# Optimization experiments

Hardware: AMD Instinct MI355X
Metric: run time of the kernel (lower is better)

Reference implementation:

```python
import jax, jax.numpy as jnp
import numpy as np
from jax import lax

B, N = 4, 192
D_IN = 768       # bert hidden
H = 512          # lstm_hid_size (bidirectional)
HD = H // 2
DIST_E = 20
TYPE_E = 20
CONV_IN = H + DIST_E + TYPE_E   # 552
CONV_H = 96
DILATIONS = (1, 2, 3)
BIAFF = 512
CLS = 10
N_POS = 30
SIZE_E = 25


def setup_inputs() -> dict:
    key = jax.random.key(0)
    ks = iter(jax.random.split(key, 48))

    def nrm(shape, s):
        return jax.random.normal(next(ks), shape, jnp.float32) * s

    word_reps = jax.random.normal(next(ks), (B, N, D_IN), jnp.float32)
    word_length = jnp.concatenate([
        jnp.array([N], jnp.int32),
        jax.random.randint(next(ks), (B - 1,), N // 2, N + 1).astype(jnp.int32)])
    dist_inputs = jax.random.randint(next(ks), (B, N, N), 0, 20)
    ar = jnp.arange(N)
    valid = (ar[None, :, None] < word_length[:, None, None]) & (ar[None, None, :] < word_length[:, None, None])
    loss_mask = valid.astype(jnp.int32)
    return dict(
        word_reps=word_reps, word_length=word_length, dist_inputs=dist_inputs, loss_mask=loss_mask,
        lstm_Wih_f=nrm((4 * HD, D_IN), 0.03), lstm_Whh_f=nrm((4 * HD, HD), 0.03), lstm_b_f=jnp.zeros((4 * HD,), jnp.float32),
        lstm_Wih_b=nrm((4 * HD, D_IN), 0.03), lstm_Whh_b=nrm((4 * HD, HD), 0.03), lstm_b_b=jnp.zeros((4 * HD,), jnp.float32),
        cln_gamma=jnp.ones((H,), jnp.float32), cln_beta=jnp.zeros((H,), jnp.float32),
        cln_Wg=nrm((H, H), 0.02), cln_Wb=nrm((H, H), 0.02),
        dis_emb=nrm((20, DIST_E), 0.1), reg_emb=nrm((3, TYPE_E), 0.1),
        conv_base_w=nrm((1, 1, CONV_IN, CONV_H), 0.05), conv_base_b=jnp.zeros((CONV_H,), jnp.float32),
        conv_dw_w=nrm((len(DILATIONS), 3, 3, 1, CONV_H), 0.05), conv_dw_b=jnp.zeros((len(DILATIONS), CONV_H), jnp.float32),
        mlp1_w=nrm((BIAFF, H), 0.04), mlp1_b=jnp.zeros((BIAFF,), jnp.float32),
        mlp2_w=nrm((BIAFF, H), 0.04), mlp2_b=jnp.zeros((BIAFF,), jnp.float32),
        head_w=nrm((BIAFF, H), 0.04), head_b=jnp.zeros((BIAFF,), jnp.float32),
        tail_w=nrm((BIAFF, H), 0.04), tail_b=jnp.zeros((BIAFF,), jnp.float32),
        biaff_W=nrm((CLS, BIAFF + 1, BIAFF + 1), 0.02),
        size_emb=nrm((N_POS, SIZE_E), 0.1),
        W_co=nrm((CLS, 2 * (BIAFF + 1) + SIZE_E), 0.02),
    )


def _lstm_dir(x, mask, Wih, Whh, b):
    # x: [B,T,D], mask: [B,T] bool. PyTorch LSTM (packed): padded steps emit 0, state frozen.
    xw = jnp.einsum('btd,gd->btg', x, Wih) + b  # precomputed input projection, gate order i,f,g,o
    h0 = jnp.zeros((x.shape[0], Whh.shape[1]), x.dtype)

    def step(carry, inp):
        h, c = carry
        xw_t, m_t = inp
        gates = xw_t + h @ Whh.T
        i, f, g, o = jnp.split(gates, 4, axis=-1)
        c_new = jax.nn.sigmoid(f) * c + jax.nn.sigmoid(i) * jnp.tanh(g)
        h_new = jax.nn.sigmoid(o) * jnp.tanh(c_new)
        m = m_t[:, None]
        h = jnp.where(m, h_new, h)
        c = jnp.where(m, c_new, c)
        return (h, c), jnp.where(m, h_new, 0.0)

    _, hs = lax.scan(step, (h0, h0), (xw.transpose(1, 0, 2), mask.T))
    return hs.transpose(1, 0, 2)


def _conv2d_nhwc(x, w, b, dil, groups):
    pad = (w.shape[0] - 1) // 2 * dil
    y = lax.conv_general_dilated(
        x, w, window_strides=(1, 1), padding=[(pad, pad), (pad, pad)],
        rhs_dilation=(dil, dil),
        dimension_numbers=('NHWC', 'HWIO', 'NHWC'),
        feature_group_count=groups)
    return y + b


def _forward(word_reps, lstm_Wih_f, lstm_Whh_f, lstm_b_f, lstm_Wih_b, lstm_Whh_b, lstm_b_b,
             cln_gamma, cln_beta, cln_Wg, cln_Wb, dis_emb, reg_emb,
             conv_base_w, conv_base_b, conv_dw_w, conv_dw_b,
             mlp1_w, mlp1_b, mlp2_w, mlp2_b, head_w, head_b, tail_w, tail_b,
             biaff_W, size_emb, W_co,
             word_length, dist_inputs, loss_mask):
    Bsz, T, _ = word_reps.shape
    ar = jnp.arange(T)
    seq_mask = ar[None, :] < word_length[:, None]

    # --- BiLSTM over packed (length-masked) sequences ---
    fwd = _lstm_dir(word_reps, seq_mask, lstm_Wih_f, lstm_Whh_f, lstm_b_f)
    idx = jnp.clip(word_length[:, None] - 1 - ar[None, :], 0, T - 1)  # reverse within each length
    x_rev = jnp.take_along_axis(word_reps, idx[:, :, None], axis=1)
    bwd_rev = _lstm_dir(x_rev, seq_mask, lstm_Wih_b, lstm_Whh_b, lstm_b_b)
    bwd = jnp.take_along_axis(bwd_rev, idx[:, :, None], axis=1) * seq_mask[:, :, None]
    wr = jnp.concatenate([fwd, bwd], axis=-1)  # [B,T,H]

    # --- conditional LayerNorm: normalize wr[i], scale/shift conditioned on wr[j] ---
    mu = wr.mean(-1, keepdims=True)
    xc = wr - mu
    var = (xc * xc).mean(-1, keepdims=True)
    ln = xc / jnp.sqrt(var + 1e-12)                 # [B,T,H]
    w_cond = cln_gamma + wr @ cln_Wg.T              # [B,T,H]
    b_cond = cln_beta + wr @ cln_Wb.T
    cln = ln[:, :, None, :] * w_cond[:, None, :, :] + b_cond[:, None, :, :]  # [B,T,T,H]

    dis = dis_emb[dist_inputs]                      # [B,T,T,20]
    reg_inputs = jnp.tril(loss_mask) + loss_mask    # values in {0,1,2}
    reg = reg_emb[reg_inputs]                       # [B,T,T,20]
    grid_mask = (loss_mask != 0)[..., None]
    conv_in = jnp.where(grid_mask, jnp.concatenate([dis, reg, cln], axis=-1), 0.0)

    # --- dilated depthwise conv stack (act='leakyrelu') ---
    x = jax.nn.leaky_relu(_conv2d_nhwc(conv_in, conv_base_w, conv_base_b, 1, 1))
    outs = []
    for i, d in enumerate(DILATIONS):
        x = jax.nn.leaky_relu(_conv2d_nhwc(x, conv_dw_w[i], conv_dw_b[i], d, CONV_H))
        outs.append(x)
    conv_out = jnp.where(grid_mask, jnp.concatenate(outs, axis=-1), 0.0)
    del conv_out  # computed in source, but CoPredictor.forward ignores z (faithful)

    # --- CoPredictor ---
    gelu = lambda v: jax.nn.gelu(v, approximate=False)
    h = gelu(wr @ mlp1_w.T + mlp1_b)
    t = gelu(wr @ mlp2_w.T + mlp2_b)
    ones = jnp.ones(h.shape[:-1] + (1,), h.dtype)
    h1 = jnp.concatenate([h, ones], -1)
    t1 = jnp.concatenate([t, ones], -1)
    o1 = jnp.einsum('bxi,oij,byj->bxyo', h1, biaff_W, t1)  # [B,T,T,CLS]

    head = jnp.concatenate([jax.nn.leaky_relu(wr @ head_w.T + head_b), ones], -1)  # [B,T,P]
    tail = jnp.concatenate([jax.nn.leaky_relu(wr @ tail_w.T + tail_b), ones], -1)
    span = ar[None, :] - ar[:, None]
    span = jnp.clip(span, -(N_POS // 2), N_POS // 2 - 1) + N_POS // 2
    se = size_emb[span]  # [T,T,SIZE_E]
    P = BIAFF + 1
    # einsum over the concat [head|tail|size] split into three partial products (no [B,T,T,1051] materialization)
    o3 = (jnp.einsum('bmi,ki->bkm', head, W_co[:, :P])[:, :, :, None]
          + jnp.einsum('bni,ki->bkn', tail, W_co[:, P:2 * P])[:, :, None, :]
          + jnp.einsum('mns,ks->kmn', se, W_co[:, 2 * P:])[None])
    return jnp.transpose(o1, (0, 3, 1, 2)) + o3  # [B,CLS,T,T]


def reference(word_reps, word_length, dist_inputs, loss_mask,
              lstm_Wih_f, lstm_Whh_f, lstm_b_f, lstm_Wih_b, lstm_Whh_b, lstm_b_b,
              cln_gamma, cln_beta, cln_Wg, cln_Wb, dis_emb, reg_emb,
              conv_base_w, conv_base_b, conv_dw_w, conv_dw_b,
              mlp1_w, mlp1_b, mlp2_w, mlp2_b, head_w, head_b, tail_w, tail_b,
              biaff_W, size_emb, W_co):
    return _forward(word_reps, lstm_Wih_f, lstm_Whh_f, lstm_b_f, lstm_Wih_b, lstm_Whh_b, lstm_b_b,
                    cln_gamma, cln_beta, cln_Wg, cln_Wb, dis_emb, reg_emb,
                    conv_base_w, conv_base_b, conv_dw_w, conv_dw_b,
                    mlp1_w, mlp1_b, mlp2_w, mlp2_b, head_w, head_b, tail_w, tail_b,
                    biaff_W, size_emb, W_co,
                    word_length, dist_inputs, loss_mask)
```

## Files before the change

kernel.cpp:

```cpp
#include <hip/hip_runtime.h>
#include <math.h>

#define BB 4
#define NN 192
#define DIN 768
#define HD 256
#define HH 512
#define PP 513
#define CLS 10
#define NBIG 5130
#define KP 544
#define WCO_LD 1051
#define LMAX 192

typedef __attribute__((ext_vector_type(8))) __bf16 bf16x8;
typedef __attribute__((ext_vector_type(4))) float f32x4;
typedef unsigned short u16;
typedef unsigned long long u64;

__device__ __forceinline__ float sigf(float x) { return 1.f / (1.f + expf(-x)); }

__device__ __forceinline__ u16 f2bf(float f) {
    unsigned int x = __float_as_uint(f);
    unsigned int r = (x + 0x7FFF + ((x >> 16) & 1)) >> 16;
    return (u16)r;
}
__device__ __forceinline__ float bf2f(u16 h) {
    return __uint_as_float(((unsigned int)h) << 16);
}

__global__ void split_hl(const float* __restrict__ src, u16* __restrict__ hi,
                         u16* __restrict__ lo, int n)
{
    int i = blockIdx.x * blockDim.x + threadIdx.x;
    if (i >= n) return;
    float v = src[i];
    u16 h = f2bf(v);
    hi[i] = h;
    lo[i] = f2bf(v - bf2f(h));
}

__global__ void split_ht(const float* __restrict__ HT, u16* __restrict__ h1h,
                         u16* __restrict__ h1l, u16* __restrict__ t1h,
                         u16* __restrict__ t1l)
{
    int idx = blockIdx.x * blockDim.x + threadIdx.x;
    if (idx >= 768 * KP) return;
    int m = idx / KP, k = idx - m * KP;
    float hv = (k < 512) ? HT[(size_t)m * 2048 + k] : (k == 512 ? 1.f : 0.f);
    float tv = (k < 512) ? HT[(size_t)m * 2048 + 512 + k] : (k == 512 ? 1.f : 0.f);
    u16 hh = f2bf(hv);
    h1h[idx] = hh; h1l[idx] = f2bf(hv - bf2f(hh));
    u16 th = f2bf(tv);
    t1h[idx] = th; t1l[idx] = f2bf(tv - bf2f(th));
}

__global__ void wsplit_kernel(const float* __restrict__ W, u16* __restrict__ Wh,
                              u16* __restrict__ Wl)
{
    __shared__ float tile[32][33];
    int kc = blockIdx.z, k0 = blockIdx.x * 32, j0 = blockIdx.y * 32;
    int tx = threadIdx.x, ty = threadIdx.y;
#pragma unroll
    for (int yy = 0; yy < 32; yy += 8) {
        int k = k0 + ty + yy, j = j0 + tx;
        tile[ty + yy][tx] = (k < 513 && j < 513) ? W[((size_t)kc * 513 + k) * 513 + j] : 0.f;
    }
    __syncthreads();
#pragma unroll
    for (int yy = 0; yy < 32; yy += 8) {
        int j = j0 + ty + yy, k = k0 + tx;
        if (j < 513 && k < KP) {
            float v = tile[tx][ty + yy];
            size_t o = ((size_t)kc * 513 + j) * KP + k;
            u16 h = f2bf(v);
            Wh[o] = h; Wl[o] = f2bf(v - bf2f(h));
        }
    }
}

__global__ __launch_bounds__(256)
void gemm_mfma_hl(const u16* __restrict__ Ah, const u16* __restrict__ Al,
                  const u16* __restrict__ Bh, const u16* __restrict__ Bl,
                  const float* __restrict__ bias, float* __restrict__ C,
                  int K, int ldc, int act)
{
    const int lane = threadIdx.x & 63, w = threadIdx.x >> 6;
    const int m0 = blockIdx.y * 64;
    const int n0 = blockIdx.x * 64 + w * 16;
    const int arow = m0 + (lane & 15);
    const int brow = n0 + (lane & 15);
    const int koff = (lane >> 4) * 8;
    f32x4 acc[4] = {};

    for (int k0 = 0; k0 < K; k0 += 32) {
        bf16x8 bh = *(const bf16x8*)(Bh + (size_t)brow * K + k0 + koff);
        bf16x8 bl = *(const bf16x8*)(Bl + (size_t)brow * K + k0 + koff);
#pragma unroll
        for (int mi = 0; mi < 4; ++mi) {
            size_t ao = (size_t)(arow + mi * 16) * K + k0 + koff;
            bf16x8 ah = *(const bf16x8*)(Ah + ao);
            bf16x8 al = *(const bf16x8*)(Al + ao);
            acc[mi] = __builtin_amdgcn_mfma_f32_16x16x32_bf16(ah, bh, acc[mi], 0, 0, 0);
            acc[mi] = __builtin_amdgcn_mfma_f32_16x16x32_bf16(ah, bl, acc[mi], 0, 0, 0);
            acc[mi] = __builtin_amdgcn_mfma_f32_16x16x32_bf16(al, bh, acc[mi], 0, 0, 0);
        }
    }
    const float bv = bias ? bias[n0 + (lane & 15)] : 0.f;
    const int cn = n0 + (lane & 15);
#pragma unroll
    for (int mi = 0; mi < 4; ++mi)
#pragma unroll
        for (int r = 0; r < 4; ++r) {
            int m = m0 + mi * 16 + (lane >> 4) * 4 + r;
            float v = acc[mi][r] + bv;
            if (act == 1) v = 0.5f * v * (1.f + erff(v * 0.70710678118654752f));
            else if (act == 2) v = v > 0.f ? v : 0.01f * v;
            C[(size_t)m * ldc + cn] = v;
        }
}

__global__ __launch_bounds__(256)
void biaff_mfma(const u16* __restrict__ Ah, const u16* __restrict__ Al,
                const u16* __restrict__ Wh, const u16* __restrict__ Wl,
                u16* __restrict__ Mh, u16* __restrict__ Ml)
{
    const int lane = threadIdx.x & 63, w = threadIdx.x >> 6;
    const int m0 = blockIdx.y * 64;
    const int n0 = blockIdx.x * 128 + w * 32;
    const int arow = m0 + (lane & 15);
    const int koff = (lane >> 4) * 8;
    f32x4 acc[4][2] = {};

    for (int c = 0; c < 17; ++c) {
        const int k0 = c * 32 + koff;
        bf16x8 bh[2], bl[2];
#pragma unroll
        for (int ni = 0; ni < 2; ++ni) {
            size_t bo = (size_t)(n0 + ni * 16 + (lane & 15)) * KP + k0;
            bh[ni] = *(const bf16x8*)(Wh + bo);
            bl[ni] = *(const bf16x8*)(Wl + bo);
        }
#pragma unroll
        for (int mi = 0; mi < 4; ++mi) {
            size_t ao = (size_t)(arow + mi * 16) * KP + k0;
            bf16x8 ah = *(const bf16x8*)(Ah + ao);
            bf16x8 al = *(const bf16x8*)(Al + ao);
#pragma unroll
            for (int ni = 0; ni < 2; ++ni) {
                acc[mi][ni] = __builtin_amdgcn_mfma_f32_16x16x32_bf16(ah, bh[ni], acc[mi][ni], 0, 0, 0);
                acc[mi][ni] = __builtin_amdgcn_mfma_f32_16x16x32_bf16(ah, bl[ni], acc[mi][ni], 0, 0, 0);
                acc[mi][ni] = __builtin_amdgcn_mfma_f32_16x16x32_bf16(al, bh[ni], acc[mi][ni], 0, 0, 0);
            }
        }
    }
#pragma unroll
    for (int mi = 0; mi < 4; ++mi)
#pragma unroll
        for (int ni = 0; ni < 2; ++ni) {
            int n = n0 + ni * 16 + (lane & 15);
            if (n < NBIG) {
                int kc = n / PP, j = n - kc * PP;
#pragma unroll
                for (int r = 0; r < 4; ++r) {
                    int m = m0 + mi * 16 + (lane >> 4) * 4 + r;
                    float v = acc[mi][ni][r];
                    u16 h = f2bf(v);
                    size_t o = (size_t)m * (CLS * KP) + kc * KP + j;
                    Mh[o] = h; Ml[o] = f2bf(v - bf2f(h));
                }
            }
        }
}

__global__ __launch_bounds__(256)
void final_mfma(const u16* __restrict__ Mh, const u16* __restrict__ Ml,
                const u16* __restrict__ Th, const u16* __restrict__ Tl,
                const float* __restrict__ hv, const float* __restrict__ tv,
                const float* __restrict__ Tt, float* __restrict__ out)
{
    const int lane = threadIdx.x & 63, w = threadIdx.x >> 6;
    const int r0 = blockIdx.y * 64;
    const int b = r0 / 1920;
    const int rem = r0 - b * 1920;
    const int kc = rem / 192;
    const int x0 = rem - kc * 192;
    const int n0 = blockIdx.x * 64 + w * 16;
    const int koff = (lane >> 4) * 8;
    const size_t abase = (size_t)(b * 192 + x0 + (lane & 15)) * (CLS * KP) + kc * KP;
    const size_t bbase = (size_t)(b * 192 + n0 + (lane & 15)) * KP;
    f32x4 acc[4] = {};

    for (int c = 0; c < 17; ++c) {
        const int k0 = c * 32 + koff;
        bf16x8 bh = *(const bf16x8*)(Th + bbase + k0);
        bf16x8 bl = *(const bf16x8*)(Tl + bbase + k0);
#pragma unroll
        for (int mi = 0; mi < 4; ++mi) {
            size_t ao = abase + (size_t)mi * 16 * (CLS * KP) + k0;
            bf16x8 ah = *(const bf16x8*)(Mh + ao);
            bf16x8 al = *(const bf16x8*)(Ml + ao);
            acc[mi] = __builtin_amdgcn_mfma_f32_16x16x32_bf16(ah, bh, acc[mi], 0, 0, 0);
            acc[mi] = __builtin_amdgcn_mfma_f32_16x16x32_bf16(ah, bl, acc[mi], 0, 0, 0);
            acc[mi] = __builtin_amdgcn_mfma_f32_16x16x32_bf16(al, bh, acc[mi], 0, 0, 0);
        }
    }
    const int bk = b * 10 + kc;
    const int y = n0 + (lane & 15);
    const float tvv = tv[bk * 192 + y];
#pragma unroll
    for (int mi = 0; mi < 4; ++mi)
#pragma unroll
        for (int r = 0; r < 4; ++r) {
            int x = x0 + mi * 16 + (lane >> 4) * 4 + r;
            int d = y - x;
            d = d < -15 ? -15 : (d > 14 ? 14 : d);
            float v = acc[mi][r] + hv[bk * 192 + x] + tvv + Tt[kc * 30 + d + 15];
            out[(size_t)(bk * 192 + x) * 192 + y] = v;
        }
}

__global__ void pack_w(const float* __restrict__ Wf, const float* __restrict__ Wb,
                       u16* __restrict__ pw)
{
    int f = blockIdx.x * blockDim.x + threadIdx.x;
    if (f >= 4 * 8 * 32 * 64 * 8) return;
    int e = f & 7;
    int lane = (f >> 3) & 63;
    int frag = (f >> 9) & 31;
    int wave = (f >> 14) & 7;
    int dh = f >> 17;
    int dir = dh >> 1, half = dh & 1;
    int kt = frag >> 2, t = frag & 3;
    int col = half * 512 + wave * 64 + t * 16 + (lane & 15);
    int u = col >> 2, gt = col & 3;
    int g = gt * 256 + u;
    int k = kt * 32 + (lane >> 4) * 8 + e;
    const float* W = dir ? Wb : Wf;
    pw[f] = f2bf(W[g * 256 + k]);
}

__global__ __launch_bounds__(512, 2)
void lstm_mfma(const float* __restrict__ xw, const u16* __restrict__ pw,
               const int* __restrict__ wl, float* __restrict__ wr,
               u64* __restrict__ ex)
{
    const int dh = blockIdx.x;
    const int dir = dh >> 1, half = dh & 1;
    const int tid = threadIdx.x;
    const int lane = tid & 63, wid = tid >> 6;

    __shared__ __align__(16) u16 h_hi[16 * 256];
    __shared__ __align__(16) u16 h_lo[16 * 256];
    __shared__ __align__(16) float gates_s[512 * 4];

    for (int i = tid; i < 16 * 256; i += 512) { h_hi[i] = 0; h_lo[i] = 0; }

    bf16x8 bw[32];
    {
        const u16* base = pw + ((size_t)(dh * 8 + wid) * 32 * 64 + lane) * 8;
#pragma unroll
        for (int i = 0; i < 32; ++i)
            bw[i] = *reinterpret_cast<const bf16x8*>(base + (size_t)i * 64 * 8);
    }

    const int u_loc = tid >> 2, bb = tid & 3;
    const int u_glob = half * 128 + u_loc;
    const int Lb = wl[bb];
    float c_state = 0.f, h_state = 0.f;

    const int row = lane & 15, quad = lane >> 4;
    const int abase = row * 512 + quad * 16;
    const int aswz = (row & 7) << 4;
    const int wswz = bb << 4;

    __syncthreads();

    f32x4 acc[4];
    for (int t = 0; t < LMAX; ++t) {
        int ttok = (dir == 0) ? t : (Lb - 1 - t);
        if (ttok < 0) ttok = 0;
        const float* xrow = xw + ((size_t)(bb * 192 + ttok)) * 2048 + dir * 1024 + u_glob;
        float x0 = xrow[0], x1 = xrow[256], x2 = xrow[512], x3 = xrow[768];

#pragma unroll
        for (int tt = 0; tt < 4; ++tt)
#pragma unroll
            for (int e = 0; e < 4; ++e) acc[tt][e] = 0.f;
#pragma unroll
        for (int kt = 0; kt < 8; ++kt) {
            int off = (abase + kt * 64) ^ aswz;
            bf16x8 ah = *reinterpret_cast<const bf16x8*>((const char*)h_hi + off);
            bf16x8 al = *reinterpret_cast<const bf16x8*>((const char*)h_lo + off);
#pragma unroll
            for (int tt = 0; tt < 4; ++tt) {
                acc[tt] = __builtin_amdgcn_mfma_f32_16x16x32_bf16(ah, bw[kt * 4 + tt], acc[tt], 0, 0, 0);
                acc[tt] = __builtin_amdgcn_mfma_f32_16x16x32_bf16(al, bw[kt * 4 + tt], acc[tt], 0, 0, 0);
            }
        }
        if (lane < 16) {
#pragma unroll
            for (int tt = 0; tt < 4; ++tt) {
                int col_loc = wid * 64 + tt * 16 + lane;
                *reinterpret_cast<f32x4*>(&gates_s[col_loc * 4]) = acc[tt];
            }
        }
        __syncthreads();

        float gi = gates_s[(u_loc * 4 + 0) * 4 + bb] + x0;
        float gf = gates_s[(u_loc * 4 + 1) * 4 + bb] + x1;
        float gg = gates_s[(u_loc * 4 + 2) * 4 + bb] + x2;
        float go = gates_s[(u_loc * 4 + 3) * 4 + bb] + x3;
        float cn = sigf(gf) * c_state + sigf(gi) * tanhf(gg);
        float hn = sigf(go) * tanhf(cn);
        if (t < Lb) {
            c_state = cn; h_state = hn;
            wr[((size_t)(bb * 192 + ttok)) * 512 + dir * 256 + u_glob] = hn;
        }
        u16 hi_b = f2bf(h_state);
        u16 lo_b = f2bf(h_state - bf2f(hi_b));
        {
            int lb = (bb * 512 + u_glob * 2) ^ wswz;
            *(u16*)((char*)h_hi + lb) = hi_b;
            *(u16*)((char*)h_lo + lb) = lo_b;
        }
        unsigned int packv = ((unsigned int)lo_b << 16) | hi_b;

        u64 vv = (u64)packv | ((u64)(unsigned int)(t + 1) << 32);
        __hip_atomic_store(&ex[((size_t)dh * 2 + (t & 1)) * 512 + tid], vv,
                           __ATOMIC_RELAXED, __HIP_MEMORY_SCOPE_AGENT);
        u64 pv;
        do {
            pv = __hip_atomic_load(&ex[((size_t)(dh ^ 1) * 2 + (t & 1)) * 512 + tid],
                                   __ATOMIC_RELAXED, __HIP_MEMORY_SCOPE_AGENT);
            if ((unsigned int)(pv >> 32) == (unsigned int)(t + 1)) break;
            __builtin_amdgcn_s_sleep(1);
        } while (true);
        {
            unsigned int pk = (unsigned int)pv;
            int pu = (half ^ 1) * 128 + (tid >> 2);
            int lb = (bb * 512 + pu * 2) ^ wswz;
            *(u16*)((char*)h_hi + lb) = (u16)(pk & 0xFFFFu);
            *(u16*)((char*)h_lo + lb) = (u16)(pk >> 16);
        }
        __syncthreads();
    }
}

__global__ __launch_bounds__(192)
void hvtv_kernel(const float* __restrict__ HT, const float* __restrict__ Wco,
                 float* __restrict__ hv, float* __restrict__ tv)
{
    int bk = blockIdx.x;
    int b = bk / 10, k = bk - (bk / 10) * 10;
    int x = threadIdx.x;
    const float* hrow = HT + (size_t)(b * 192 + x) * 2048 + 1024;
    const float* trow = hrow + 512;
    const float* wk = Wco + k * WCO_LD;
    float sh = wk[512], st = wk[1025];
    for (int i = 0; i < 512; ++i) {
        sh = fmaf(hrow[i], wk[i], sh);
        st = fmaf(trow[i], wk[513 + i], st);
    }
    hv[bk * 192 + x] = sh;
    tv[bk * 192 + x] = st;
}

__global__ void ttab_kernel(const float* __restrict__ size_emb,
                            const float* __restrict__ Wco, float* __restrict__ Tt)
{
    int idx = blockIdx.x * blockDim.x + threadIdx.x;
    if (idx >= 300) return;
    int k = idx / 30, p = idx - (idx / 30) * 30;
    float s = 0.f;
    for (int e = 0; e < 25; ++e)
        s = fmaf(size_emb[p * 25 + e], Wco[k * WCO_LD + 1026 + e], s);
    Tt[idx] = s;
}

extern "C" void kernel_launch(void* const* d_in, const int* in_sizes, int n_in,
                              void* d_out, int out_size, void* d_ws, size_t ws_size,
                              hipStream_t stream)
{
    const float* word_reps = (const float*)d_in[0];
    const int*   word_length = (const int*)d_in[1];
    const float* Wih_f = (const float*)d_in[4];
    const float* Whh_f = (const float*)d_in[5];
    const float* b_f   = (const float*)d_in[6];
    const float* Wih_b = (const float*)d_in[7];
    const float* Whh_b = (const float*)d_in[8];
    const float* b_b   = (const float*)d_in[9];
    const float* mlp1_w = (const float*)d_in[20];
    const float* mlp1_b = (const float*)d_in[21];
    const float* mlp2_w = (const float*)d_in[22];
    const float* mlp2_b = (const float*)d_in[23];
    const float* head_w = (const float*)d_in[24];
    const float* head_b = (const float*)d_in[25];
    const float* tail_w = (const float*)d_in[26];
    const float* tail_b = (const float*)d_in[27];
    const float* biaffW = (const float*)d_in[28];
    const float* size_emb = (const float*)d_in[29];
    const float* W_co = (const float*)d_in[30];

    float* W = (float*)d_ws;
    float* xw   = W;
    u16*   pw   = (u16*)(W + 1572864);
    float* wr   = W + 1835008;
    u16*   Mbh  = (u16*)W;
    float* HT   = W + 2228224;
    u16* h1h = (u16*)(W + 3801088);
    u16* h1l = (u16*)(W + 4009984);
    u16* t1h = (u16*)(W + 4218880);
    u16* t1l = (u16*)(W + 4427776);
    u16* Wsph = (u16*)(W + 4636672);
    u16* Wspl = (u16*)(W + 6064128);
    u16* Mbl  = (u16*)(W + 7491584);
    float* hv = W + 9580544;
    float* tv = W + 9588224;
    float* Tt = W + 9595904;
    u64* ex   = (u64*)(W + 9596208);
    u16* wrph = (u16*)(W + 9604400);
    u16* wrpl = (u16*)(W + 9899312);
    u16* wihh = (u16*)(W + 10194224);
    u16* wihl = (u16*)(W + 10587440);
    u16* wrsh = (u16*)(W + 10980656);
    u16* wrsl = (u16*)(W + 11177264);
    u16* mwh  = (u16*)(W + 11373872);
    u16* mwl  = (u16*)(W + 11504944);

    hipMemsetAsync(wr, 0, (size_t)393216 * 4, stream);
    hipMemsetAsync(ex, 0, (size_t)4096 * 8, stream);
    hipMemsetAsync(Wsph, 0, (size_t)2 * 2854912 * 2, stream);

    pack_w<<<(4 * 8 * 32 * 64 * 8 + 255) / 256, 256, 0, stream>>>(Whh_f, Whh_b, pw);
    wsplit_kernel<<<dim3(17, 17, 10), dim3(32, 8), 0, stream>>>(biaffW, Wsph, Wspl);

    split_hl<<<(589824 + 255) / 256, 256, 0, stream>>>(word_reps, wrph, wrpl, 589824);
    split_hl<<<(786432 + 255) / 256, 256, 0, stream>>>(Wih_f, wihh, wihl, 786432);
    gemm_mfma_hl<<<dim3(16, 12), 256, 0, stream>>>(wrph, wrpl, wihh, wihl, b_f, xw, 768, 2048, 0);
    split_hl<<<(786432 + 255) / 256, 256, 0, stream>>>(Wih_b, wihh, wihl, 786432);
    gemm_mfma_hl<<<dim3(16, 12), 256, 0, stream>>>(wrph, wrpl, wihh, wihl, b_b, xw + 1024, 768, 2048, 0);

    lstm_mfma<<<4, 512, 0, stream>>>(xw, pw, word_length, wr, ex);

    split_hl<<<(393216 + 255) / 256, 256, 0, stream>>>(wr, wrsh, wrsl, 393216);
    split_hl<<<(262144 + 255) / 256, 256, 0, stream>>>(mlp1_w, mwh, mwl, 262144);
    gemm_mfma_hl<<<dim3(8, 12), 256, 0, stream>>>(wrsh, wrsl, mwh, mwl, mlp1_b, HT, 512, 2048, 1);
    split_hl<<<(262144 + 255) / 256, 256, 0, stream>>>(mlp2_w, mwh, mwl, 262144);
    gemm_mfma_hl<<<dim3(8, 12), 256, 0, stream>>>(wrsh, wrsl, mwh, mwl, mlp2_b, HT + 512, 512, 2048, 1);
    split_hl<<<(262144 + 255) / 256, 256, 0, stream>>>(head_w, mwh, mwl, 262144);
    gemm_mfma_hl<<<dim3(8, 12), 256, 0, stream>>>(wrsh, wrsl, mwh, mwl, head_b, HT + 1024, 512, 2048, 2);
    split_hl<<<(262144 + 255) / 256, 256, 0, stream>>>(tail_w, mwh, mwl, 262144);
    gemm_mfma_hl<<<dim3(8, 12), 256, 0, stream>>>(wrsh, wrsl, mwh, mwl, tail_b, HT + 1536, 512, 2048, 2);

    split_ht<<<(768 * KP + 255) / 256, 256, 0, stream>>>(HT, h1h, h1l, t1h, t1l);
    hvtv_kernel<<<40, 192, 0, stream>>>(HT, W_co, hv, tv);
    ttab_kernel<<<2, 256, 0, stream>>>(size_emb, W_co, Tt);

    hipMemsetAsync(Mbh, 0, (size_t)4177920 * 2, stream);
    hipMemsetAsync(Mbl, 0, (size_t)4177920 * 2, stream);

    biaff_mfma<<<dim3(41, 12), 256, 0, stream>>>(h1h, h1l, Wsph, Wspl, Mbh, Mbl);
    final_mfma<<<dim3(3, 120), 256, 0, stream>>>(Mbh, Mbl, t1h, t1l, hv, tv, Tt, (float*)d_out);
}
```

Baseline: 826.0 us.

## Fuse prep splits, batch GEMMs, and overlap LSTM cross-block exchange

All fp32-to-bf16 hi/lo splits, the Whh packing and the bias concatenation are merged into one prep kernel. The two input-projection GEMMs become one launch, and so do the four MLP GEMMs, with the activation chosen per column. The LSTM recurrence now keeps a single interleaved hi/lo h buffer in shared memory. It computes the local half of the K dimension before waiting on the partner block, prefetches the next step's x, polls with LLC-bypassing loads, and writes bf16 hi/lo outputs directly so the later split is no longer needed. The hv/tv and Ttab kernels are merged and parallelised with wave reductions. The risks are the spin-wait protocol, which has a timeout break, and the workspace aliasing being reorganised.

```diff
diff --git a/kernel.cpp b/kernel.cpp
--- a/kernel.cpp
+++ b/kernel.cpp
@@ -16,43 +16,92 @@
 typedef __attribute__((ext_vector_type(8))) __bf16 bf16x8;
 typedef __attribute__((ext_vector_type(4))) float f32x4;
 typedef unsigned short u16;
+typedef unsigned int u32;
 typedef unsigned long long u64;
 
 __device__ __forceinline__ float sigf(float x) { return 1.f / (1.f + expf(-x)); }
 
 __device__ __forceinline__ u16 f2bf(float f) {
-    unsigned int x = __float_as_uint(f);
-    unsigned int r = (x + 0x7FFF + ((x >> 16) & 1)) >> 16;
+    u32 x = __float_as_uint(f);
+    u32 r = (x + 0x7FFF + ((x >> 16) & 1)) >> 16;
     return (u16)r;
 }
 __device__ __forceinline__ float bf2f(u16 h) {
-    return __uint_as_float(((unsigned int)h) << 16);
-}
-
-__global__ void split_hl(const float* __restrict__ src, u16* __restrict__ hi,
-                         u16* __restrict__ lo, int n)
+    return __uint_as_float(((u32)h) << 16);
+}
+
+__device__ __forceinline__ u64 ld_llc(const u64* p) {
+    u64 r;
+    asm volatile("global_load_dwordx2 %0, %1, off sc0 sc1\n\ts_waitcnt vmcnt(0)"
+                 : "=v"(r) : "v"(p) : "memory");
+    return r;
+}
+
+__global__ void mega_prep(const float* __restrict__ word_reps,
+                          const float* __restrict__ Wih_f, const float* __restrict__ Wih_b,
+                          const float* __restrict__ b_f, const float* __restrict__ b_b,
+                          const float* __restrict__ mlp1_w, const float* __restrict__ mlp2_w,
+                          const float* __restrict__ head_w, const float* __restrict__ tail_w,
+                          const float* __restrict__ mlp1_b, const float* __restrict__ mlp2_b,
+                          const float* __restrict__ head_b, const float* __restrict__ tail_b,
+                          const float* __restrict__ Whh_f, const float* __restrict__ Whh_b,
+                          u16* __restrict__ wrph, u16* __restrict__ wrpl,
+                          u16* __restrict__ wihh, u16* __restrict__ wihl, float* __restrict__ bias_ih,
+                          u16* __restrict__ mwh, u16* __restrict__ mwl, float* __restrict__ bias_mid,
+                          u16* __restrict__ pw)
 {
     int i = blockIdx.x * blockDim.x + threadIdx.x;
-    if (i >= n) return;
-    float v = src[i];
-    u16 h = f2bf(v);
-    hi[i] = h;
-    lo[i] = f2bf(v - bf2f(h));
-}
-
-__global__ void split_ht(const float* __restrict__ HT, u16* __restrict__ h1h,
-                         u16* __restrict__ h1l, u16* __restrict__ t1h,
-                         u16* __restrict__ t1l)
-{
-    int idx = blockIdx.x * blockDim.x + threadIdx.x;
-    if (idx >= 768 * KP) return;
-    int m = idx / KP, k = idx - m * KP;
-    float hv = (k < 512) ? HT[(size_t)m * 2048 + k] : (k == 512 ? 1.f : 0.f);
-    float tv = (k < 512) ? HT[(size_t)m * 2048 + 512 + k] : (k == 512 ? 1.f : 0.f);
-    u16 hh = f2bf(hv);
-    h1h[idx] = hh; h1l[idx] = f2bf(hv - bf2f(hh));
-    u16 th = f2bf(tv);
-    t1h[idx] = th; t1l[idx] = f2bf(tv - bf2f(th));
+    if (i < 589824) {
+        float v = word_reps[i];
+        u16 h = f2bf(v);
+        wrph[i] = h; wrpl[i] = f2bf(v - bf2f(h));
+        return;
+    }
+    i -= 589824;
+    if (i < 1572864) {
+        int n = i / 768, k = i - n * 768;
+        float v = (n < 1024) ? Wih_f[(size_t)n * 768 + k] : Wih_b[(size_t)(n - 1024) * 768 + k];
+        u16 h = f2bf(v);
+        wihh[i] = h; wihl[i] = f2bf(v - bf2f(h));
+        return;
+    }
+    i -= 1572864;
+    if (i < 1048576) {
+        int n = i >> 9, k = i & 511;
+        const float* Ws = (n < 512) ? mlp1_w : (n < 1024) ? mlp2_w : (n < 1536) ? head_w : tail_w;
+        float v = Ws[(size_t)(n & 511) * 512 + k];
+        u16 h = f2bf(v);
+        mwh[i] = h; mwl[i] = f2bf(v - bf2f(h));
+        return;
+    }
+    i -= 1048576;
+    if (i < 524288) {
+        int f = i;
+        int e = f & 7;
+        int lane = (f >> 3) & 63;
+        int frag = (f >> 9) & 31;
+        int wave = (f >> 14) & 7;
+        int dh = f >> 17;
+        int dir = dh >> 1, half = dh & 1;
+        int kt = frag >> 2, t = frag & 3;
+        int col = half * 512 + wave * 64 + t * 16 + (lane & 15);
+        int u = col >> 2, gt = col & 3;
+        int g = gt * 256 + u;
+        int k = kt * 32 + (lane >> 4) * 8 + e;
+        const float* W = dir ? Whh_b : Whh_f;
+        pw[f] = f2bf(W[(size_t)g * 256 + k]);
+        return;
+    }
+    i -= 524288;
+    if (i < 2048) {
+        bias_ih[i] = (i < 1024) ? b_f[i] : b_b[i - 1024];
+        return;
+    }
+    i -= 2048;
+    if (i < 2048) {
+        bias_mid[i] = (i < 512) ? mlp1_b[i] : (i < 1024) ? mlp2_b[i - 512]
+                    : (i < 1536) ? head_b[i - 1024] : tail_b[i - 1536];
+    }
 }
 
 __global__ void wsplit_kernel(const float* __restrict__ W, u16* __restrict__ Wh,
@@ -106,16 +155,17 @@
             acc[mi] = __builtin_amdgcn_mfma_f32_16x16x32_bf16(al, bh, acc[mi], 0, 0, 0);
         }
     }
-    const float bv = bias ? bias[n0 + (lane & 15)] : 0.f;
     const int cn = n0 + (lane & 15);
+    const float bv = bias ? bias[cn] : 0.f;
+    const int am = (act == 3) ? (cn < 1024 ? 1 : 2) : act;
 #pragma unroll
     for (int mi = 0; mi < 4; ++mi)
 #pragma unroll
         for (int r = 0; r < 4; ++r) {
             int m = m0 + mi * 16 + (lane >> 4) * 4 + r;
             float v = acc[mi][r] + bv;
-            if (act == 1) v = 0.5f * v * (1.f + erff(v * 0.70710678118654752f));
-            else if (act == 2) v = v > 0.f ? v : 0.01f * v;
+            if (am == 1) v = 0.5f * v * (1.f + erff(v * 0.70710678118654752f));
+            else if (am == 2) v = v > 0.f ? v : 0.01f * v;
             C[(size_t)m * ldc + cn] = v;
         }
 }
@@ -220,29 +270,9 @@
         }
 }
 
-__global__ void pack_w(const float* __restrict__ Wf, const float* __restrict__ Wb,
-                       u16* __restrict__ pw)
-{
-    int f = blockIdx.x * blockDim.x + threadIdx.x;
-    if (f >= 4 * 8 * 32 * 64 * 8) return;
-    int e = f & 7;
-    int lane = (f >> 3) & 63;
-    int frag = (f >> 9) & 31;
-    int wave = (f >> 14) & 7;
-    int dh = f >> 17;
-    int dir = dh >> 1, half = dh & 1;
-    int kt = frag >> 2, t = frag & 3;
-    int col = half * 512 + wave * 64 + t * 16 + (lane & 15);
-    int u = col >> 2, gt = col & 3;
-    int g = gt * 256 + u;
-    int k = kt * 32 + (lane >> 4) * 8 + e;
-    const float* W = dir ? Wb : Wf;
-    pw[f] = f2bf(W[g * 256 + k]);
-}
-
 __global__ __launch_bounds__(512, 2)
 void lstm_mfma(const float* __restrict__ xw, const u16* __restrict__ pw,
-               const int* __restrict__ wl, float* __restrict__ wr,
+               const int* __restrict__ wl, u16* __restrict__ wrsh, u16* __restrict__ wrsl,
                u64* __restrict__ ex)
 {
     const int dh = blockIdx.x;
@@ -250,11 +280,10 @@
     const int tid = threadIdx.x;
     const int lane = tid & 63, wid = tid >> 6;
 
-    __shared__ __align__(16) u16 h_hi[16 * 256];
-    __shared__ __align__(16) u16 h_lo[16 * 256];
-    __shared__ __align__(16) float gates_s[512 * 4];
-
-    for (int i = tid; i < 16 * 256; i += 512) { h_hi[i] = 0; h_lo[i] = 0; }
+    __shared__ __align__(16) u16 h_s[16 * 256];
+    __shared__ __align__(16) float gates_s[512 * 8];
+
+    for (int i = tid; i < 16 * 256; i += 512) h_s[i] = 0;
 
     bf16x8 bw[32];
     {
@@ -272,110 +301,155 @@
     const int row = lane & 15, quad = lane >> 4;
     const int abase = row * 512 + quad * 16;
     const int aswz = (row & 7) << 4;
-    const int wswz = bb << 4;
+    const int swzh = (bb & 7) << 4;
+    const int swzl = ((bb + 4) & 7) << 4;
+
+    u64* my = ex + (size_t)dh * 1024 + tid;
+    const u64* pa = ex + (size_t)(dh ^ 1) * 1024 + tid;
+
+    const int kl0 = half * 4;
+    const int kr0 = (1 - half) * 4;
 
     __syncthreads();
 
+    int tt0 = dir ? (Lb - 1) : 0; if (tt0 < 0) tt0 = 0;
+    const float* xr = xw + ((size_t)(bb * 192 + tt0)) * 2048 + dir * 1024 + u_glob;
+    float x0 = xr[0], x1 = xr[256], x2 = xr[512], x3 = xr[768];
+
+    bool fast = true;
     f32x4 acc[4];
     for (int t = 0; t < LMAX; ++t) {
-        int ttok = (dir == 0) ? t : (Lb - 1 - t);
-        if (ttok < 0) ttok = 0;
-        const float* xrow = xw + ((size_t)(bb * 192 + ttok)) * 2048 + dir * 1024 + u_glob;
-        float x0 = xrow[0], x1 = xrow[256], x2 = xrow[512], x3 = xrow[768];
-
-#pragma unroll
-        for (int tt = 0; tt < 4; ++tt)
-#pragma unroll
-            for (int e = 0; e < 4; ++e) acc[tt][e] = 0.f;
-#pragma unroll
-        for (int kt = 0; kt < 8; ++kt) {
+        int ttn = dir ? (Lb - 2 - t) : (t + 1);
+        if (ttn < 0) ttn = 0; if (ttn > 191) ttn = 191;
+        const float* xrn = xw + ((size_t)(bb * 192 + ttn)) * 2048 + dir * 1024 + u_glob;
+        float nx0 = xrn[0], nx1 = xrn[256], nx2 = xrn[512], nx3 = xrn[768];
+
+#pragma unroll
+        for (int tt = 0; tt < 4; ++tt) acc[tt] = (f32x4){0.f, 0.f, 0.f, 0.f};
+#pragma unroll
+        for (int k2 = 0; k2 < 4; ++k2) {
+            const int kt = kl0 + k2;
             int off = (abase + kt * 64) ^ aswz;
-            bf16x8 ah = *reinterpret_cast<const bf16x8*>((const char*)h_hi + off);
-            bf16x8 al = *reinterpret_cast<const bf16x8*>((const char*)h_lo + off);
+            bf16x8 a = *reinterpret_cast<const bf16x8*>((const char*)h_s + off);
+#pragma unroll
+            for (int tt = 0; tt < 4; ++tt)
+                acc[tt] = __builtin_amdgcn_mfma_f32_16x16x32_bf16(a, bw[kt * 4 + tt], acc[tt], 0, 0, 0);
+        }
+
+        if (t > 0) {
+            const u64* pp = pa + (t & 1) * 512;
+            u64 pv; int spin = 0;
+            for (;;) {
+                pv = fast ? ld_llc(pp)
+                          : __hip_atomic_load(pp, __ATOMIC_RELAXED, __HIP_MEMORY_SCOPE_AGENT);
+                if ((u32)(pv >> 32) == (u32)t) break;
+                if (++spin == 4096) fast = false;
+                if (spin > 50000000) break;
+            }
+            u32 pk = (u32)pv;
+            int pu = (half ^ 1) * 128 + u_loc;
+            *(u16*)((char*)h_s + ((bb * 512 + pu * 2) ^ swzh)) = (u16)(pk & 0xFFFFu);
+            *(u16*)((char*)h_s + (((bb + 4) * 512 + pu * 2) ^ swzl)) = (u16)(pk >> 16);
+        }
+        __syncthreads();
+
+#pragma unroll
+        for (int k2 = 0; k2 < 4; ++k2) {
+            const int kt = kr0 + k2;
+            int off = (abase + kt * 64) ^ aswz;
+            bf16x8 a = *reinterpret_cast<const bf16x8*>((const char*)h_s + off);
+#pragma unroll
+            for (int tt = 0; tt < 4; ++tt)
+                acc[tt] = __builtin_amdgcn_mfma_f32_16x16x32_bf16(a, bw[kt * 4 + tt], acc[tt], 0, 0, 0);
+        }
+        if (lane < 32) {
 #pragma unroll
             for (int tt = 0; tt < 4; ++tt) {
-                acc[tt] = __builtin_amdgcn_mfma_f32_16x16x32_bf16(ah, bw[kt * 4 + tt], acc[tt], 0, 0, 0);
-                acc[tt] = __builtin_amdgcn_mfma_f32_16x16x32_bf16(al, bw[kt * 4 + tt], acc[tt], 0, 0, 0);
-            }
-        }
-        if (lane < 16) {
-#pragma unroll
-            for (int tt = 0; tt < 4; ++tt) {
-                int col_loc = wid * 64 + tt * 16 + lane;
-                *reinterpret_cast<f32x4*>(&gates_s[col_loc * 4]) = acc[tt];
+                int col_loc = wid * 64 + tt * 16 + (lane & 15);
+                *reinterpret_cast<f32x4*>(&gates_s[col_loc * 8 + quad * 4]) = acc[tt];
             }
         }
         __syncthreads();
 
-        float gi = gates_s[(u_loc * 4 + 0) * 4 + bb] + x0;
-        float gf = gates_s[(u_loc * 4 + 1) * 4 + bb] + x1;
-        float gg = gates_s[(u_loc * 4 + 2) * 4 + bb] + x2;
-        float go = gates_s[(u_loc * 4 + 3) * 4 + bb] + x3;
+        const float* gs = &gates_s[u_loc * 32];
+        float gi = gs[0 + bb]  + gs[4 + bb]  + x0;
+        float gf = gs[8 + bb]  + gs[12 + bb] + x1;
+        float gg = gs[16 + bb] + gs[20 + bb] + x2;
+        float go = gs[24 + bb] + gs[28 + bb] + x3;
         float cn = sigf(gf) * c_state + sigf(gi) * tanhf(gg);
         float hn = sigf(go) * tanhf(cn);
+        if (t < Lb) { c_state = cn; h_state = hn; }
+        u16 hb = f2bf(h_state);
+        u16 lb = f2bf(h_state - bf2f(hb));
+
+        u64 vv = (u64)(((u32)lb << 16) | hb) | ((u64)(u32)(t + 1) << 32);
+        __hip_atomic_store(my + ((t + 1) & 1) * 512, vv,
+                           __ATOMIC_RELAXED, __HIP_MEMORY_SCOPE_AGENT);
+
         if (t < Lb) {
-            c_state = cn; h_state = hn;
-            wr[((size_t)(bb * 192 + ttok)) * 512 + dir * 256 + u_glob] = hn;
-        }
-        u16 hi_b = f2bf(h_state);
-        u16 lo_b = f2bf(h_state - bf2f(hi_b));
-        {
-            int lb = (bb * 512 + u_glob * 2) ^ wswz;
-            *(u16*)((char*)h_hi + lb) = hi_b;
-            *(u16*)((char*)h_lo + lb) = lo_b;
-        }
-        unsigned int packv = ((unsigned int)lo_b << 16) | hi_b;
-
-        u64 vv = (u64)packv | ((u64)(unsigned int)(t + 1) << 32);
-        __hip_atomic_store(&ex[((size_t)dh * 2 + (t & 1)) * 512 + tid], vv,
-                           __ATOMIC_RELAXED, __HIP_MEMORY_SCOPE_AGENT);
-        u64 pv;
-        do {
-            pv = __hip_atomic_load(&ex[((size_t)(dh ^ 1) * 2 + (t & 1)) * 512 + tid],
-                                   __ATOMIC_RELAXED, __HIP_MEMORY_SCOPE_AGENT);
-            if ((unsigned int)(pv >> 32) == (unsigned int)(t + 1)) break;
-            __builtin_amdgcn_s_sleep(1);
-        } while (true);
-        {
-            unsigned int pk = (unsigned int)pv;
-            int pu = (half ^ 1) * 128 + (tid >> 2);
-            int lb = (bb * 512 + pu * 2) ^ wswz;
-            *(u16*)((char*)h_hi + lb) = (u16)(pk & 0xFFFFu);
-            *(u16*)((char*)h_lo + lb) = (u16)(pk >> 16);
-        }
+            int ttok = dir ? (Lb - 1 - t) : t;
+            size_t wo = ((size_t)(bb * 192 + ttok)) * 512 + dir * 256 + u_glob;
+            wrsh[wo] = hb; wrsl[wo] = lb;
+        }
+        *(u16*)((char*)h_s + ((bb * 512 + u_glob * 2) ^ swzh)) = hb;
+        *(u16*)((char*)h_s + (((bb + 4) * 512 + u_glob * 2) ^ swzl)) = lb;
+        x0 = nx0; x1 = nx1; x2 = nx2; x3 = nx3;
         __syncthreads();
     }
 }
 
-__global__ __launch_bounds__(192)
-void hvtv_kernel(const float* __restrict__ HT, const float* __restrict__ Wco,
-                 float* __restrict__ hv, float* __restrict__ tv)
+__global__ void split_ht(const float* __restrict__ HT, u16* __restrict__ h1h,
+                         u16* __restrict__ h1l, u16* __restrict__ t1h,
+                         u16* __restrict__ t1l)
+{
+    int idx = blockIdx.x * blockDim.x + threadIdx.x;
+    if (idx >= 768 * KP) return;
+    int m = idx / KP, k = idx - m * KP;
+    float hv = (k < 512) ? HT[(size_t)m * 2048 + k] : (k == 512 ? 1.f : 0.f);
+    float tv = (k < 512) ? HT[(size_t)m * 2048 + 512 + k] : (k == 512 ? 1.f : 0.f);
+    u16 hh = f2bf(hv);
+    h1h[idx] = hh; h1l[idx] = f2bf(hv - bf2f(hh));
+    u16 th = f2bf(tv);
+    t1h[idx] = th; t1l[idx] = f2bf(tv - bf2f(th));
+}
+
+__global__ __launch_bounds__(256)
+void hvtv_ttab(const float* __restrict__ HT, const float* __restrict__ Wco,
+               const float* __restrict__ size_emb,
+               float* __restrict__ hv, float* __restrict__ tv, float* __restrict__ Tt)
 {
     int bk = blockIdx.x;
-    int b = bk / 10, k = bk - (bk / 10) * 10;
-    int x = threadIdx.x;
-    const float* hrow = HT + (size_t)(b * 192 + x) * 2048 + 1024;
-    const float* trow = hrow + 512;
-    const float* wk = Wco + k * WCO_LD;
-    float sh = wk[512], st = wk[1025];
-    for (int i = 0; i < 512; ++i) {
-        sh = fmaf(hrow[i], wk[i], sh);
-        st = fmaf(trow[i], wk[513 + i], st);
-    }
-    hv[bk * 192 + x] = sh;
-    tv[bk * 192 + x] = st;
-}
-
-__global__ void ttab_kernel(const float* __restrict__ size_emb,
-                            const float* __restrict__ Wco, float* __restrict__ Tt)
-{
-    int idx = blockIdx.x * blockDim.x + threadIdx.x;
-    if (idx >= 300) return;
-    int k = idx / 30, p = idx - (idx / 30) * 30;
-    float s = 0.f;
-    for (int e = 0; e < 25; ++e)
-        s = fmaf(size_emb[p * 25 + e], Wco[k * WCO_LD + 1026 + e], s);
-    Tt[idx] = s;
+    if (bk < 40) {
+        int b = bk / 10, k = bk - (bk / 10) * 10;
+        int wave = threadIdx.x >> 6, lane = threadIdx.x & 63;
+        const float* wk = Wco + k * WCO_LD;
+        for (int x = wave; x < 192; x += 4) {
+            const float* hrow = HT + (size_t)(b * 192 + x) * 2048 + 1024;
+            float sh = 0.f, st = 0.f;
+            for (int i = lane; i < 512; i += 64) {
+                sh = fmaf(hrow[i], wk[i], sh);
+                st = fmaf(hrow[512 + i], wk[513 + i], st);
+            }
+#pragma unroll
+            for (int o = 32; o; o >>= 1) {
+                sh += __shfl_down(sh, o);
+                st += __shfl_down(st, o);
+            }
+            if (lane == 0) {
+                hv[bk * 192 + x] = sh + wk[512];
+                tv[bk * 192 + x] = st + wk[1025];
+            }
+        }
+    } else {
+        int idx = (bk - 40) * 256 + threadIdx.x;
+        if (idx < 300) {
+            int k = idx / 30, p = idx - (idx / 30) * 30;
+            float s = 0.f;
+            for (int e = 0; e < 25; ++e)
+                s = fmaf(size_emb[p * 25 + e], Wco[k * WCO_LD + 1026 + e], s);
+            Tt[idx] = s;
+        }
+    }
 }
 
 extern "C" void kernel_launch(void* const* d_in, const int* in_sizes, int n_in,
@@ -404,9 +478,10 @@
 
     float* W = (float*)d_ws;
     float* xw   = W;
-    u16*   pw   = (u16*)(W + 1572864);
-    float* wr   = W + 1835008;
-    u16*   Mbh  = (u16*)W;
+    u16*  wrsh  = (u16*)(W + 1572864);
+    u16*  wrsl  = (u16*)(W + 1769472);
+    u16*  pw    = (u16*)(W + 1966080);
+    u16*  Mbh   = (u16*)W;
     float* HT   = W + 2228224;
     u16* h1h = (u16*)(W + 3801088);
     u16* h1l = (u16*)(W + 4009984);
@@ -415,47 +490,38 @@
     u16* Wsph = (u16*)(W + 4636672);
     u16* Wspl = (u16*)(W + 6064128);
     u16* Mbl  = (u16*)(W + 7491584);
+    u16* wihh = (u16*)(W + 7491584);
+    u16* wihl = (u16*)(W + 8278016);
+    float* bias_ih = W + 9064448;
     float* hv = W + 9580544;
     float* tv = W + 9588224;
     float* Tt = W + 9595904;
     u64* ex   = (u64*)(W + 9596208);
     u16* wrph = (u16*)(W + 9604400);
     u16* wrpl = (u16*)(W + 9899312);
-    u16* wihh = (u16*)(W + 10194224);
-    u16* wihl = (u16*)(W + 10587440);
-    u16* wrsh = (u16*)(W + 10980656);
-    u16* wrsl = (u16*)(W + 11177264);
-    u16* mwh  = (u16*)(W + 11373872);
-    u16* mwl  = (u16*)(W + 11504944);
-
-    hipMemsetAsync(wr, 0, (size_t)393216 * 4, stream);
+    u16* mwh  = (u16*)(W + 10194224);
+    u16* mwl  = (u16*)(W + 10718512);
+    float* bias_mid = W + 11242800;
+
+    hipMemsetAsync(wrsh, 0, (size_t)393216 * 2 * sizeof(u16), stream);
     hipMemsetAsync(ex, 0, (size_t)4096 * 8, stream);
-    hipMemsetAsync(Wsph, 0, (size_t)2 * 2854912 * 2, stream);
-
-    pack_w<<<(4 * 8 * 32 * 64 * 8 + 255) / 256, 256, 0, stream>>>(Whh_f, Whh_b, pw);
+
+    mega_prep<<<(3739648 + 255) / 256, 256, 0, stream>>>(
+        word_reps, Wih_f, Wih_b, b_f, b_b,
+        mlp1_w, mlp2_w, head_w, tail_w, mlp1_b, mlp2_b, head_b, tail_b,
+        Whh_f, Whh_b,
+        wrph, wrpl, wihh, wihl, bias_ih, mwh, mwl, bias_mid, pw);
+
     wsplit_kernel<<<dim3(17, 17, 10), dim3(32, 8), 0, stream>>>(biaffW, Wsph, Wspl);
 
-    split_hl<<<(589824 + 255) / 256, 256, 0, stream>>>(word_reps, wrph, wrpl, 589824);
-    split_hl<<<(786432 + 255) / 256, 256, 0, stream>>>(Wih_f, wihh, wihl, 786432);
-    gemm_mfma_hl<<<dim3(16, 12), 256, 0, stream>>>(wrph, wrpl, wihh, wihl, b_f, xw, 768, 2048, 0);
-    split_hl<<<(786432 + 255) / 256, 256, 0, stream>>>(Wih_b, wihh, wihl, 786432);
-    gemm_mfma_hl<<<dim3(16, 12), 256, 0, stream>>>(wrph, wrpl, wihh, wihl, b_b, xw + 1024, 768, 2048, 0);
-
-    lstm_mfma<<<4, 512, 0, stream>>>(xw, pw, word_length, wr, ex);
-
-    split_hl<<<(393216 + 255) / 256, 256, 0, stream>>>(wr, wrsh, wrsl, 393216);
-    split_hl<<<(262144 + 255) / 256, 256, 0, stream>>>(mlp1_w, mwh, mwl, 262144);
-    gemm_mfma_hl<<<dim3(8, 12), 256, 0, stream>>>(wrsh, wrsl, mwh, mwl, mlp1_b, HT, 512, 2048, 1);
-    split_hl<<<(262144 + 255) / 256, 256, 0, stream>>>(mlp2_w, mwh, mwl, 262144);
-    gemm_mfma_hl<<<dim3(8, 12), 256, 0, stream>>>(wrsh, wrsl, mwh, mwl, mlp2_b, HT + 512, 512, 2048, 1);
-    split_hl<<<(262144 + 255) / 256, 256, 0, stream>>>(head_w, mwh, mwl, 262144);
-    gemm_mfma_hl<<<dim3(8, 12), 256, 0, stream>>>(wrsh, wrsl, mwh, mwl, head_b, HT + 1024, 512, 2048, 2);
-    split_hl<<<(262144 + 255) / 256, 256, 0, stream>>>(tail_w, mwh, mwl, 262144);
-    gemm_mfma_hl<<<dim3(8, 12), 256, 0, stream>>>(wrsh, wrsl, mwh, mwl, tail_b, HT + 1536, 512, 2048, 2);
+    gemm_mfma_hl<<<dim3(32, 12), 256, 0, stream>>>(wrph, wrpl, wihh, wihl, bias_ih, xw, 768, 2048, 0);
+
+    lstm_mfma<<<4, 512, 0, stream>>>(xw, pw, word_length, wrsh, wrsl, ex);
+
+    gemm_mfma_hl<<<dim3(32, 12), 256, 0, stream>>>(wrsh, wrsl, mwh, mwl, bias_mid, HT, 512, 2048, 3);
 
     split_ht<<<(768 * KP + 255) / 256, 256, 0, stream>>>(HT, h1h, h1l, t1h, t1l);
-    hvtv_kernel<<<40, 192, 0, stream>>>(HT, W_co, hv, tv);
-    ttab_kernel<<<2, 256, 0, stream>>>(size_emb, W_co, Tt);
+    hvtv_ttab<<<42, 256, 0, stream>>>(HT, W_co, size_emb, hv, tv, Tt);
 
     hipMemsetAsync(Mbh, 0, (size_t)4177920 * 2, stream);
     hipMemsetAsync(Mbl, 0, (size_t)4177920 * 2, stream);
```

After: 2.040 ms. 2.47x slower.
